# Optimization experiments

Measured on AMD Instinct MI355X. Metric: run time of the kernel, lower is better.

## Reference

```python
import jax, jax.numpy as jnp
import numpy as np

K = 8          # number of TR cores / modes
D = 1024       # categories per mode
R = 64         # TR rank
NDRAWS = 2048
EPS = 1e-30


def setup_inputs() -> dict:
    key = jax.random.key(0)
    ks = jax.random.split(key, K)
    inp = {f"log_core{i}": jax.random.normal(ks[i], (D, R, R), dtype=jnp.float32)
           for i in range(K)}
    inp["n_draws"] = NDRAWS
    return inp


def _sample(cores, n_draws, seed=1):
    """Batched version of trip_index_sample: all draws sampled in parallel."""
    k = len(cores)
    # heads[j] = S_0 @ ... @ S_{j-1} with S_i = core_i.sum(0); heads[0] = None
    heads = [None]
    acc = cores[0].sum(axis=0)
    for c in cores[1:]:
        heads.append(acc)
        acc = acc @ c.sum(axis=0)
    norm = acc  # S_0 ... S_{K-1}

    keys = jax.random.split(jax.random.key(seed), k)
    tail = None          # [B, r_{j+1}, r_K] running suffix product per draw
    idxs = []
    for step, j in enumerate(range(k - 1, -1, -1)):
        core, head = cores[j], heads[j]
        if tail is None:
            # first step (j = K-1): marginal weights shared by all draws
            if head is None:  # degenerate K == 1 case
                w = jnp.trace(core, axis1=1, axis2=2)
            else:
                w = jnp.einsum('ab,nba->n', head, core)
            ix = jax.random.categorical(keys[step], jnp.log(jnp.clip(w, EPS)),
                                        shape=(n_draws,))
            tail = core[ix]  # [B, r_j, r_K]
        else:
            # M = tail @ head : [B, r_{j+1}, r_j] (head is None only at j == 0,
            # where r_0 == r_K so tail already has the right shape)
            M = tail if head is None else tail @ head
            w = jnp.einsum('nab,Bba->Bn', core, M)  # [B, d_j]
            ix = jax.random.categorical(keys[step], jnp.log(jnp.clip(w, EPS)),
                                        axis=-1)
            tail = jnp.einsum('Bab,Bbc->Bac', core[ix], tail)
        idxs.append(ix)
    sample = jnp.stack(idxs[::-1], axis=1)  # [B, K], mode order 0..K-1
    log_p = jnp.log(jnp.clip(jnp.trace(tail, axis1=1, axis2=2), EPS)) \
            - jnp.log(jnp.trace(norm))
    return sample, log_p


def reference(log_core0, log_core1, log_core2, log_core3,
              log_core4, log_core5, log_core6, log_core7, n_draws):
    log_cores = [log_core0, log_core1, log_core2, log_core3,
                 log_core4, log_core5, log_core6, log_core7]
    cores = [jax.nn.softplus(c) for c in log_cores]
    sample, log_p = _sample(cores, n_draws)
    return sample, log_p
```

## Files before the change

kernel.cpp:

```cpp
#include <hip/hip_runtime.h>
#include <stdint.h>
#include <math.h>

#define D_CAT  1024
#define R_TR   64
#define RR     4096
#define NDRAWS 2048
#define KMODES 8

struct CorePtrs { const float* p[KMODES]; };

typedef __attribute__((ext_vector_type(8))) __bf16 bf16x8;
typedef __attribute__((ext_vector_type(4))) float  f32x4;
typedef unsigned int u32;

union BF8 { ushort u[8]; bf16x8 v; };

static __device__ inline void async_cp16(const void* g, void* l) {
  __builtin_amdgcn_global_load_lds(
      (const __attribute__((address_space(1))) u32*)g,
      (__attribute__((address_space(3))) u32*)l, 16, 0, 0);
}

static __host__ __device__ inline uint32_t rotl32(uint32_t x, int r) {
  return (x << r) | (x >> (32 - r));
}
static __host__ __device__ inline void tf2x32(uint32_t k1, uint32_t k2,
                                              uint32_t x0, uint32_t x1,
                                              uint32_t& o0, uint32_t& o1) {
  uint32_t ks0 = k1, ks1 = k2, ks2 = k1 ^ k2 ^ 0x1BD11BDAu;
  x0 += ks0; x1 += ks1;
  x0 += x1; x1 = rotl32(x1, 13); x1 ^= x0;
  x0 += x1; x1 = rotl32(x1, 15); x1 ^= x0;
  x0 += x1; x1 = rotl32(x1, 26); x1 ^= x0;
  x0 += x1; x1 = rotl32(x1, 6);  x1 ^= x0;
  x0 += ks1; x1 += ks2 + 1u;
  x0 += x1; x1 = rotl32(x1, 17); x1 ^= x0;
  x0 += x1; x1 = rotl32(x1, 29); x1 ^= x0;
  x0 += x1; x1 = rotl32(x1, 16); x1 ^= x0;
  x0 += x1; x1 = rotl32(x1, 24); x1 ^= x0;
  x0 += ks2; x1 += ks0 + 2u;
  x0 += x1; x1 = rotl32(x1, 13); x1 ^= x0;
  x0 += x1; x1 = rotl32(x1, 15); x1 ^= x0;
  x0 += x1; x1 = rotl32(x1, 26); x1 ^= x0;
  x0 += x1; x1 = rotl32(x1, 6);  x1 ^= x0;
  x0 += ks0; x1 += ks1 + 3u;
  x0 += x1; x1 = rotl32(x1, 17); x1 ^= x0;
  x0 += x1; x1 = rotl32(x1, 29); x1 ^= x0;
  x0 += x1; x1 = rotl32(x1, 16); x1 ^= x0;
  x0 += x1; x1 = rotl32(x1, 24); x1 ^= x0;
  x0 += ks1; x1 += ks2 + 4u;
  x0 += x1; x1 = rotl32(x1, 13); x1 ^= x0;
  x0 += x1; x1 = rotl32(x1, 15); x1 ^= x0;
  x0 += x1; x1 = rotl32(x1, 26); x1 ^= x0;
  x0 += x1; x1 = rotl32(x1, 6);  x1 ^= x0;
  x0 += ks2; x1 += ks0 + 5u;
  o0 = x0; o1 = x1;
}

static __device__ inline float softplus_fast(float x) {
  float e = __expf(-fabsf(x));
  return fmaxf(x, 0.0f) + __logf(1.0f + e);
}

static __device__ inline unsigned short f32_bf16(float f) {
  uint32_t u = __float_as_uint(f);
  u += 0x7fffu + ((u >> 16) & 1u);
  return (unsigned short)(u >> 16);
}

static __device__ inline float gumbel_at(uint32_t k1, uint32_t k2, uint32_t e) {
  uint32_t o0, o1;
  tf2x32(k1, k2, 0u, e, o0, o1);
  uint32_t bits = o0 ^ o1;
  float f = __uint_as_float((bits >> 9) | 0x3F800000u) - 1.0f;
  float u = (f > 0.0f) ? f : 1.17549435e-38f;
  return -logf(-logf(u));
}


__global__ void k_sentinel(float* out, int n) {
  int i = blockIdx.x * 256 + threadIdx.x;
  if (i < n) out[i] = -12288.0f;
}

__global__ __launch_bounds__(256) void k_spart(CorePtrs cp, float* __restrict__ Spart) {
  const int bid = blockIdx.x, tid = threadIdx.x;
  const int i = bid >> 8, c = bid & 255;
  const float* src = cp.p[i] + (size_t)c * 4 * RR;
  float acc[16];
#pragma unroll
  for (int k = 0; k < 16; ++k) acc[k] = 0.0f;
#pragma unroll
  for (int d = 0; d < 4; ++d) {
    const float* row = src + (size_t)d * RR;
#pragma unroll
    for (int k = 0; k < 16; ++k)
      acc[k] += softplus_fast(row[tid + k * 256]);
  }
  float* dst = Spart + (size_t)bid * RR;
#pragma unroll
  for (int k = 0; k < 16; ++k) dst[tid + k * 256] = acc[k];
}

__global__ __launch_bounds__(256) void k_sreduce(const float* __restrict__ Spart,
                                                 double* __restrict__ S) {
  const int idx = blockIdx.x * 256 + threadIdx.x;
  const int i = idx >> 12, rr = idx & 4095;
  const float* p = Spart + ((size_t)i << 20) + rr;
  double a0 = 0.0, a1 = 0.0, a2 = 0.0, a3 = 0.0;
  for (int c = 0; c < 256; c += 4) {
    a0 += (double)p[(size_t)(c + 0) * RR];
    a1 += (double)p[(size_t)(c + 1) * RR];
    a2 += (double)p[(size_t)(c + 2) * RR];
    a3 += (double)p[(size_t)(c + 3) * RR];
  }
  S[idx] = (a0 + a1) + (a2 + a3);
}

__global__ __launch_bounds__(256) void k_heads(const double* __restrict__ S,
                                               double* __restrict__ heads,
                                               double* __restrict__ misc) {
  __shared__ double cur[RR];
  __shared__ double Sm[RR];
  __shared__ double tbuf[64];
  const int tid = threadIdx.x;
  const int bcol = tid & 63;
  const int a0 = tid >> 6;
#pragma unroll
  for (int k = 0; k < 16; ++k) {
    int p = tid + k * 256;
    double v = S[p];
    cur[p] = v;
    heads[p] = v;
  }
  __syncthreads();
  for (int m = 1; m <= 6; ++m) {
#pragma unroll
    for (int k = 0; k < 16; ++k) {
      int p = tid + k * 256;
      Sm[p] = S[(size_t)m * RR + p];
    }
    __syncthreads();
    double acc[16];
#pragma unroll
    for (int k = 0; k < 16; ++k) acc[k] = 0.0;
    for (int c = 0; c < 64; ++c) {
      double s = Sm[c * 64 + bcol];
#pragma unroll
      for (int k = 0; k < 16; ++k)
        acc[k] = fma(cur[(a0 + 4 * k) * 64 + c], s, acc[k]);
    }
    __syncthreads();
#pragma unroll
    for (int k = 0; k < 16; ++k) {
      int p = tid + k * 256;
      cur[p] = acc[k];
      heads[(size_t)m * RR + p] = acc[k];
    }
    __syncthreads();
  }
#pragma unroll
  for (int k = 0; k < 16; ++k) {
    int p = tid + k * 256;
    Sm[p] = S[(size_t)7 * RR + p];
  }
  __syncthreads();
  if (tid < 64) {
    double acc = 0.0;
    for (int c = 0; c < 64; ++c)
      acc = fma(cur[tid * 64 + c], Sm[c * 64 + tid], acc);
    tbuf[tid] = acc;
  }
  __syncthreads();
  if (tid == 0) {
    double tr = 0.0;
    for (int a = 0; a < 64; ++a) tr += tbuf[a];
    misc[0] = log(tr);
  }
}

__global__ __launch_bounds__(256) void k_w0(const float* __restrict__ raw,
                                            const double* __restrict__ head7,
                                            float* __restrict__ W) {
  const int tid = threadIdx.x;
  const int lane = tid & 63;
  const int n = blockIdx.x * 4 + (tid >> 6);
  const float* crow = raw + (size_t)n * RR;
  double acc = 0.0;
  for (int q = lane; q < RR; q += 64)
    acc = fma((double)softplus_fast(crow[q]), head7[(q & 63) * 64 + (q >> 6)], acc);
  for (int m = 32; m; m >>= 1) acc += __shfl_xor(acc, m);
  if (lane == 0) W[n] = (float)acc;
}

__global__ __launch_bounds__(256) void k_spmt(const float* __restrict__ src,
                                              ushort* __restrict__ Bh,
                                              ushort* __restrict__ Bl,
                                              const float* __restrict__ tail,
                                              const double* __restrict__ head, int useHead,
                                              ushort* __restrict__ Ah,
                                              ushort* __restrict__ Al) {
  __shared__ alignas(16) float smem[4176];
  const int bid = blockIdx.x, tid = threadIdx.x;
  if (bid < 4096) {
    const size_t i4 = ((size_t)bid * 256 + tid) * 4;
    float4 v = *(const float4*)(src + i4);
    const float ov[4] = {softplus_fast(v.x), softplus_fast(v.y),
                         softplus_fast(v.z), softplus_fast(v.w)};
    ushort h4[4], l4[4];
#pragma unroll
    for (int q = 0; q < 4; ++q) {
      ushort h = f32_bf16(ov[q]);
      float hf = __uint_as_float((uint32_t)h << 16);
      h4[q] = h;
      l4[q] = f32_bf16(ov[q] - hf);
    }
    *(ushort4*)(Bh + i4) = make_ushort4(h4[0], h4[1], h4[2], h4[3]);
    *(ushort4*)(Bl + i4) = make_ushort4(l4[0], l4[1], l4[2], l4[3]);
    return;
  }
  const int blk = bid - 4096;
  if (useHead) {
    ushort (*hT)[4096] = (ushort(*)[4096])smem;
#pragma unroll
    for (int rep = 0; rep < 16; ++rep) {
      int i = tid + rep * 256;
      float v = (float)head[(i & 63) * 64 + (i >> 6)];
      ushort h = f32_bf16(v);
      float hf = __uint_as_float((uint32_t)h << 16);
      int dst = (i & 0xFC0) | (((((i >> 3) & 7) ^ ((i >> 6) & 7)) << 3)) | (i & 7);
      hT[0][dst] = h;
      hT[1][dst] = f32_bf16(v - hf);
    }
    __syncthreads();
    const int w = tid >> 6, l = tid & 63;
    const int B = blk * 4 + w;
    const float* tb = tail + (size_t)B * RR;
    const int lrow = l & 15, kg = l >> 4;
    ushort* ah_out = Ah + (size_t)B * RR;
    ushort* al_out = Al + (size_t)B * RR;
    for (int it = 0; it < 4; ++it) {
      BF8 afh[2], afl[2];
#pragma unroll
      for (int kt = 0; kt < 2; ++kt) {
        const float* s2 = tb + (it * 16 + lrow) * 64 + kt * 32 + kg * 8;
        float4 v0 = *(const float4*)s2;
        float4 v1 = *(const float4*)(s2 + 4);
        float vv[8] = {v0.x, v0.y, v0.z, v0.w, v1.x, v1.y, v1.z, v1.w};
#pragma unroll
        for (int q = 0; q < 8; ++q) {
          ushort h = f32_bf16(vv[q]);
          float hf = __uint_as_float((uint32_t)h << 16);
          afh[kt].u[q] = h;
          afl[kt].u[q] = f32_bf16(vv[q] - hf);
        }
      }
#pragma unroll
      for (int kt2 = 0; kt2 < 4; ++kt2) {
        f32x4 hh = (f32x4)0.0f, sm = (f32x4)0.0f;
#pragma unroll
        for (int kt = 0; kt < 2; ++kt) {
          int rowB = kt2 * 16 + lrow;
          int kcA  = kt * 4 + kg;
          int off  = rowB * 64 + ((kcA ^ (rowB & 7)) << 3);
          bf16x8 bh = *(const bf16x8*)&hT[0][off];
          bf16x8 bl = *(const bf16x8*)&hT[1][off];
          hh = __builtin_amdgcn_mfma_f32_16x16x32_bf16(afh[kt].v, bh, hh, 0, 0, 0);
          sm = __builtin_amdgcn_mfma_f32_16x16x32_bf16(afh[kt].v, bl, sm, 0, 0, 0);
          sm = __builtin_amdgcn_mfma_f32_16x16x32_bf16(afl[kt].v, bh, sm, 0, 0, 0);
        }
        ushort h4[4], l4[4];
#pragma unroll
        for (int q = 0; q < 4; ++q) {
          float v = hh[q] + sm[q];
          ushort h = f32_bf16(v);
          float hf = __uint_as_float((uint32_t)h << 16);
          h4[q] = h;
          l4[q] = f32_bf16(v - hf);
        }
        int o = (kt2 * 16 + lrow) * 64 + it * 16 + kg * 4;
        *(ushort4*)(ah_out + o) = make_ushort4(h4[0], h4[1], h4[2], h4[3]);
        *(ushort4*)(al_out + o) = make_ushort4(l4[0], l4[1], l4[2], l4[3]);
      }
    }
  } else {
    float* tl = smem;
    for (int d = 0; d < 4; ++d) {
      const int B = blk * 4 + d;
      const float* tb = tail + (size_t)B * RR;
      ushort* ah_out = Ah + (size_t)B * RR;
      ushort* al_out = Al + (size_t)B * RR;
      __syncthreads();
#pragma unroll
      for (int r = 0; r < 4; ++r) {
        int p = tid * 4 + r * 1024;
        int i = p >> 6, k = p & 63;
        float4 v = *(const float4*)(tb + p);
        tl[i * 65 + k + 0] = v.x; tl[i * 65 + k + 1] = v.y;
        tl[i * 65 + k + 2] = v.z; tl[i * 65 + k + 3] = v.w;
      }
      __syncthreads();
#pragma unroll
      for (int r = 0; r < 4; ++r) {
        int p = tid * 4 + r * 1024;
        int k = p >> 6, i0 = p & 63;
        ushort h4[4], l4[4];
#pragma unroll
        for (int q = 0; q < 4; ++q) {
          float m = tl[(i0 + q) * 65 + k];
          ushort h = f32_bf16(m);
          float hf = __uint_as_float((uint32_t)h << 16);
          h4[q] = h;
          l4[q] = f32_bf16(m - hf);
        }
        *(ushort4*)(ah_out + p) = make_ushort4(h4[0], h4[1], h4[2], h4[3]);
        *(ushort4*)(al_out + p) = make_ushort4(l4[0], l4[1], l4[2], l4[3]);
      }
    }
  }
}

__global__ __launch_bounds__(256) void k_wgemm(const ushort* __restrict__ Ah,
                                               const ushort* __restrict__ Al,
                                               const ushort* __restrict__ Bh,
                                               const ushort* __restrict__ Bl,
                                               float* __restrict__ W) {
  __shared__ ushort lds[4 * 4096];
  const int tid = threadIdx.x;
  const int L = blockIdx.x;
  const int half = L >> 9;
  const int r = L & 511;
  const int x = r & 7, j = r >> 3;
  const int bn = (x & 1) * 8 + (j & 7);
  const int bb = (x >> 1) * 8 + (j >> 3);
  const int w = tid >> 6, l = tid & 63;

  const int srow = l >> 3;
  const int skc  = l & 7;
  const ushort* gbase;
  {
    const ushort* bases[4] = {Ah + (size_t)bb * 64 * RR, Al + (size_t)bb * 64 * RR,
                              Bh + (size_t)bn * 64 * RR, Bl + (size_t)bn * 64 * RR};
    gbase = bases[w] + (size_t)srow * RR + (size_t)((skc ^ srow) * 8)
          + (size_t)half * 2048;
  }

  const int wm = (w >> 1) * 32, wn = (w & 1) * 32;
  const int lrow = l & 15;
  const int kg   = l >> 4;

  f32x4 acc_hh[2][2], acc_sm[2][2], hht[2][2];
#pragma unroll
  for (int mt = 0; mt < 2; ++mt)
#pragma unroll
    for (int nt = 0; nt < 2; ++nt) {
      acc_hh[mt][nt] = (f32x4)0.0f;
      acc_sm[mt][nt] = (f32x4)0.0f;
      hht[mt][nt]    = (f32x4)0.0f;
    }

  int roffA[2][2], roffB[2][2];
#pragma unroll
  for (int mt = 0; mt < 2; ++mt)
#pragma unroll
    for (int kt = 0; kt < 2; ++kt) {
      int rowA = wm + mt * 16 + lrow;
      int kcA  = kt * 4 + kg;
      roffA[mt][kt] = rowA * 64 + ((kcA ^ (rowA & 7)) << 3);
      int rowB = wn + mt * 16 + lrow;
      roffB[mt][kt] = rowB * 64 + ((kcA ^ (rowB & 7)) << 3);
    }

  for (int t = 0; t < 32; ++t) {
    __syncthreads();
#pragma unroll
    for (int q = 0; q < 8; ++q)
      async_cp16(gbase + (size_t)q * 8 * RR + t * 64, &lds[w * 4096 + q * 512]);
    __syncthreads();
#pragma unroll
    for (int kt = 0; kt < 2; ++kt) {
      bf16x8 ah[2], al[2], bh[2], bl[2];
#pragma unroll
      for (int mt = 0; mt < 2; ++mt) {
        ah[mt] = *(const bf16x8*)&lds[0 * 4096 + roffA[mt][kt]];
        al[mt] = *(const bf16x8*)&lds[1 * 4096 + roffA[mt][kt]];
      }
#pragma unroll
      for (int nt = 0; nt < 2; ++nt) {
        bh[nt] = *(const bf16x8*)&lds[2 * 4096 + roffB[nt][kt]];
        bl[nt] = *(const bf16x8*)&lds[3 * 4096 + roffB[nt][kt]];
      }
#pragma unroll
      for (int mt = 0; mt < 2; ++mt)
#pragma unroll
        for (int nt = 0; nt < 2; ++nt) {
          acc_hh[mt][nt] = __builtin_amdgcn_mfma_f32_16x16x32_bf16(ah[mt], bh[nt], acc_hh[mt][nt], 0, 0, 0);
          acc_sm[mt][nt] = __builtin_amdgcn_mfma_f32_16x16x32_bf16(ah[mt], bl[nt], acc_sm[mt][nt], 0, 0, 0);
          acc_sm[mt][nt] = __builtin_amdgcn_mfma_f32_16x16x32_bf16(al[mt], bh[nt], acc_sm[mt][nt], 0, 0, 0);
        }
    }
    if ((t & 15) == 15) {
#pragma unroll
      for (int mt = 0; mt < 2; ++mt)
#pragma unroll
        for (int nt = 0; nt < 2; ++nt) {
          hht[mt][nt] += acc_hh[mt][nt];
          acc_hh[mt][nt] = (f32x4)0.0f;
        }
    }
  }

  float* Wout = W + (size_t)half * NDRAWS * D_CAT;
#pragma unroll
  for (int mt = 0; mt < 2; ++mt)
#pragma unroll
    for (int nt = 0; nt < 2; ++nt)
#pragma unroll
      for (int q = 0; q < 4; ++q) {
        int gr = bb * 64 + wm + mt * 16 + kg * 4 + q;
        int gc = bn * 64 + wn + nt * 16 + lrow;
        Wout[(size_t)gr * D_CAT + gc] = hht[mt][nt][q] + acc_sm[mt][nt][q];
      }
}

__global__ __launch_bounds__(256) void k_samptail(const float* __restrict__ W, int shared_row,
                                                  uint32_t key1, uint32_t key2,
                                                  float* __restrict__ out, int mode_j,
                                                  const float* __restrict__ raw,
                                                  const ushort* __restrict__ Bh,
                                                  const ushort* __restrict__ Bl,
                                                  float* __restrict__ tail, int first) {
  __shared__ float sv[4];
  __shared__ int   si[4];
  __shared__ int   s_m;
  __shared__ alignas(16) ushort Th[4096];
  __shared__ alignas(16) ushort Tl[4096];
  const int b = blockIdx.x, tid = threadIdx.x;

  {
    const float* w0row = W + (shared_row ? 0 : (size_t)b * D_CAT);
    const float* w1row = W + (size_t)NDRAWS * D_CAT + (size_t)b * D_CAT;
    float best = -3.4e38f; int bidx = 0x7fffffff;
    for (int k = 0; k < 4; ++k) {
      int n = tid + k * 256;
      float wv = shared_row ? w0row[n] : (w0row[n] + w1row[n]);
      float lg = logf(fmaxf(wv, 1e-30f));
      float v = gumbel_at(key1, key2, (uint32_t)(b * D_CAT + n)) + lg;
      if (v > best || (v == best && n < bidx)) { best = v; bidx = n; }
    }
    for (int m = 32; m; m >>= 1) {
      float ov = __shfl_xor(best, m);
      int   oi = __shfl_xor(bidx, m);
      if (ov > best || (ov == best && oi < bidx)) { best = ov; bidx = oi; }
    }
    if ((tid & 63) == 0) { sv[tid >> 6] = best; si[tid >> 6] = bidx; }
    __syncthreads();
    if (tid == 0) {
      for (int t = 1; t < 4; ++t)
        if (sv[t] > best || (sv[t] == best && si[t] < bidx)) { best = sv[t]; bidx = si[t]; }
      s_m = bidx;
      out[b * KMODES + mode_j] = (float)bidx;
    }
    __syncthreads();
  }
  const int m = s_m;
  float* trow = tail + (size_t)b * RR;

  if (first) {
    const float* crow = raw + (size_t)m * RR;
#pragma unroll
    for (int r = 0; r < 4; ++r) {
      float4 v = *(const float4*)(crow + tid * 4 + r * 1024);
      float4 o;
      o.x = softplus_fast(v.x); o.y = softplus_fast(v.y);
      o.z = softplus_fast(v.z); o.w = softplus_fast(v.w);
      *(float4*)(trow + tid * 4 + r * 1024) = o;
    }
    return;
  }
  const ushort* ch = Bh + (size_t)m * RR;
  const ushort* cl = Bl + (size_t)m * RR;

#pragma unroll
  for (int r = 0; r < 4; ++r) {
    int p = tid * 4 + r * 1024;
    int i = p >> 6, k = p & 63;
    float4 v = *(const float4*)(trow + p);
    float vv[4] = {v.x, v.y, v.z, v.w};
#pragma unroll
    for (int q = 0; q < 4; ++q) {
      int row = k + q;
      int dst = row * 64 + ((((i >> 3) ^ (row & 7)) << 3)) + (i & 7);
      ushort h = f32_bf16(vv[q]);
      float hf = __uint_as_float((uint32_t)h << 16);
      Th[dst] = h;
      Tl[dst] = f32_bf16(vv[q] - hf);
    }
  }
  __syncthreads();

  const int w = tid >> 6, l = tid & 63;
  const int lrow = l & 15, kg = l >> 4;
  bf16x8 ah[2], al[2];
#pragma unroll
  for (int kt = 0; kt < 2; ++kt) {
    int off = (w * 16 + lrow) * 64 + kt * 32 + kg * 8;
    ah[kt] = *(const bf16x8*)(ch + off);
    al[kt] = *(const bf16x8*)(cl + off);
  }
#pragma unroll
  for (int jt = 0; jt < 4; ++jt) {
    f32x4 hh = (f32x4)0.0f, sm = (f32x4)0.0f;
#pragma unroll
    for (int kt = 0; kt < 2; ++kt) {
      int rowB = jt * 16 + lrow;
      int kcA  = kt * 4 + kg;
      int off  = rowB * 64 + ((kcA ^ (rowB & 7)) << 3);
      bf16x8 bh = *(const bf16x8*)&Th[off];
      bf16x8 bl = *(const bf16x8*)&Tl[off];
      hh = __builtin_amdgcn_mfma_f32_16x16x32_bf16(ah[kt], bh, hh, 0, 0, 0);
      sm = __builtin_amdgcn_mfma_f32_16x16x32_bf16(ah[kt], bl, sm, 0, 0, 0);
      sm = __builtin_amdgcn_mfma_f32_16x16x32_bf16(al[kt], bh, sm, 0, 0, 0);
      sm = __builtin_amdgcn_mfma_f32_16x16x32_bf16(al[kt], bl, sm, 0, 0, 0);
    }
#pragma unroll
    for (int q = 0; q < 4; ++q)
      trow[(w * 16 + kg * 4 + q) * 64 + jt * 16 + lrow] = hh[q] + sm[q];
  }
}

__global__ __launch_bounds__(256) void k_logp(const float* __restrict__ tail,
                                              const double* __restrict__ misc,
                                              float* __restrict__ out) {
  const int b = blockIdx.x * 256 + threadIdx.x;
  double tr = 0.0;
  for (int a = 0; a < 64; ++a) tr += (double)tail[(size_t)b * RR + a * 65];
  double lp = log(fmax(tr, 1e-30)) - misc[0];
  out[NDRAWS * KMODES + b] = (float)lp;
}

extern "C" void kernel_launch(void* const* d_in, const int* in_sizes, int n_in,
                              void* d_out, int out_size, void* d_ws, size_t ws_size,
                              hipStream_t stream) {
  (void)in_sizes; (void)n_in;
  CorePtrs cp;
  for (int i = 0; i < KMODES; ++i) cp.p[i] = (const float*)d_in[i];
  float* outf = (float*)d_out;

  char* base = (char*)d_ws;
  const size_t o_w     = 0;
  const size_t o_tail  = o_w + (size_t)2 * NDRAWS * D_CAT * 4;
  const size_t o_ahl   = o_tail + (size_t)NDRAWS * RR * 4;
  const size_t o_spart = o_ahl;
  const size_t o_S     = o_ahl + (size_t)NDRAWS * RR * 4;
  const size_t o_heads = o_S + (size_t)KMODES * RR * 8;
  const size_t o_misc  = o_heads + (size_t)7 * RR * 8;
  const size_t o_bh    = o_misc + 256;
  const size_t o_bl    = o_bh + (size_t)D_CAT * RR * 2;
  const size_t NEED    = o_bl + (size_t)D_CAT * RR * 2;
  if (ws_size < NEED) {
    k_sentinel<<<(out_size + 255) / 256, 256, 0, stream>>>(outf, out_size);
    return;
  }

  float*  W     = (float*)(base + o_w);
  float*  tail  = (float*)(base + o_tail);
  ushort* Ah    = (ushort*)(base + o_ahl);
  ushort* Al    = Ah + (size_t)NDRAWS * RR;
  float*  Spart = (float*)(base + o_spart);
  double* S     = (double*)(base + o_S);
  double* heads = (double*)(base + o_heads);
  double* misc  = (double*)(base + o_misc);
  ushort* Bh    = (ushort*)(base + o_bh);
  ushort* Bl    = (ushort*)(base + o_bl);

  uint32_t kk1[KMODES], kk2[KMODES];
  for (uint32_t s = 0; s < KMODES; ++s) tf2x32(0u, 1u, 0u, s, kk1[s], kk2[s]);

  k_spart  <<<2048, 256, 0, stream>>>(cp, Spart);
  k_sreduce<<<128,  256, 0, stream>>>(Spart, S);
  k_heads  <<<1,    256, 0, stream>>>(S, heads, misc);

  for (int s = 0; s < KMODES; ++s) {
    const int j = 7 - s;
    if (s == 0) {
      k_w0<<<256, 256, 0, stream>>>(cp.p[7], heads + (size_t)6 * RR, W);
    } else {
      k_spmt<<<4608, 256, 0, stream>>>(cp.p[j], Bh, Bl, tail,
                                       j > 0 ? heads + (size_t)(j - 1) * RR : heads,
                                       j > 0 ? 1 : 0, Ah, Al);
      k_wgemm<<<1024, 256, 0, stream>>>(Ah, Al, Bh, Bl, W);
    }
    k_samptail<<<NDRAWS, 256, 0, stream>>>(W, s == 0 ? 1 : 0, kk1[s], kk2[s],
                                           outf, j, cp.p[j], Bh, Bl, tail,
                                           s == 0 ? 1 : 0);
  }
  k_logp<<<KMODES, 256, 0, stream>>>(tail, misc, outf);
}
```

Measured before the change: 880.0 us.

## Enlarge wgemm tile to 128x64 per block to halve B-operand reloads

The split-bf16 W GEMM now gives each block a 128-row by 64-column output tile instead of 64x64. Each wave computes 4x2 MFMA tiles, and the grid shrinks from 1024 to 512 blocks. The A operand (high and low) fills 4 LDS slabs and the B operand 2, so each B tile is loaded from global memory half as often and more MFMA work is done per barrier. In exchange the kernel uses more accumulator registers and LDS per block, which may lower occupancy, and half as many blocks are available to cover the GPU's compute units.

```diff
diff --git a/kernel.cpp b/kernel.cpp
--- a/kernel.cpp
+++ b/kernel.cpp
@@ -326,33 +326,33 @@
                                                const ushort* __restrict__ Bh,
                                                const ushort* __restrict__ Bl,
                                                float* __restrict__ W) {
-  __shared__ ushort lds[4 * 4096];
+  __shared__ ushort lds[6 * 4096];
   const int tid = threadIdx.x;
   const int L = blockIdx.x;
-  const int half = L >> 9;
-  const int r = L & 511;
-  const int x = r & 7, j = r >> 3;
-  const int bn = (x & 1) * 8 + (j & 7);
-  const int bb = (x >> 1) * 8 + (j >> 3);
+  const int x = L & 7, j = L >> 3;
+  const int half = j >> 5;
+  const int j2 = j & 31;
+  const int bn = (x & 1) * 8 + (j2 & 7);
+  const int bm = (x >> 1) * 4 + (j2 >> 3);
   const int w = tid >> 6, l = tid & 63;
 
   const int srow = l >> 3;
   const int skc  = l & 7;
-  const ushort* gbase;
-  {
-    const ushort* bases[4] = {Ah + (size_t)bb * 64 * RR, Al + (size_t)bb * 64 * RR,
-                              Bh + (size_t)bn * 64 * RR, Bl + (size_t)bn * 64 * RR};
-    gbase = bases[w] + (size_t)srow * RR + (size_t)((skc ^ srow) * 8)
-          + (size_t)half * 2048;
-  }
-
-  const int wm = (w >> 1) * 32, wn = (w & 1) * 32;
+  const ushort* gbaseA = (w >= 2 ? Al : Ah) + (size_t)bm * 128 * RR
+                       + (size_t)((w & 1) * 64 + srow) * RR
+                       + (size_t)(((skc ^ srow)) * 8) + (size_t)half * 2048;
+  const ushort* gbaseB0 = Bh + (size_t)bn * 64 * RR + (size_t)srow * RR
+                        + (size_t)(((skc ^ srow)) * 8) + (size_t)half * 2048;
+  const ushort* gbaseB1 = Bl + (size_t)bn * 64 * RR + (size_t)srow * RR
+                        + (size_t)(((skc ^ srow)) * 8) + (size_t)half * 2048;
+
+  const int wm = (w >> 1) * 64, wn = (w & 1) * 32;
   const int lrow = l & 15;
   const int kg   = l >> 4;
 
-  f32x4 acc_hh[2][2], acc_sm[2][2], hht[2][2];
-#pragma unroll
-  for (int mt = 0; mt < 2; ++mt)
+  f32x4 acc_hh[4][2], acc_sm[4][2], hht[4][2];
+#pragma unroll
+  for (int mt = 0; mt < 4; ++mt)
 #pragma unroll
     for (int nt = 0; nt < 2; ++nt) {
       acc_hh[mt][nt] = (f32x4)0.0f;
@@ -360,39 +360,51 @@
       hht[mt][nt]    = (f32x4)0.0f;
     }
 
-  int roffA[2][2], roffB[2][2];
-#pragma unroll
-  for (int mt = 0; mt < 2; ++mt)
+  int roffA[4][2], roffB[2][2];
+#pragma unroll
+  for (int kt = 0; kt < 2; ++kt) {
+    int kcA = kt * 4 + kg;
+#pragma unroll
+    for (int mt = 0; mt < 4; ++mt) {
+      int rowA = wm + mt * 16 + lrow;
+      roffA[mt][kt] = rowA * 64 + ((kcA ^ (rowA & 7)) << 3);
+    }
+#pragma unroll
+    for (int nt = 0; nt < 2; ++nt) {
+      int rowB = wn + nt * 16 + lrow;
+      roffB[nt][kt] = 16384 + rowB * 64 + ((kcA ^ (rowB & 7)) << 3);
+    }
+  }
+
+  for (int t = 0; t < 32; ++t) {
+    const int koff = t * 64;
+    __syncthreads();
+#pragma unroll
+    for (int q = 0; q < 8; ++q)
+      async_cp16(gbaseA + (size_t)q * 8 * RR + koff,
+                 &lds[w * 4096 + q * 512]);
+#pragma unroll
+    for (int q = 0; q < 4; ++q) {
+      const int g = w * 4 + q;
+      const ushort* gb = (g >= 8 ? gbaseB1 : gbaseB0) + (size_t)((g & 7) * 8) * RR + koff;
+      async_cp16(gb, &lds[16384 + g * 512]);
+    }
+    __syncthreads();
 #pragma unroll
     for (int kt = 0; kt < 2; ++kt) {
-      int rowA = wm + mt * 16 + lrow;
-      int kcA  = kt * 4 + kg;
-      roffA[mt][kt] = rowA * 64 + ((kcA ^ (rowA & 7)) << 3);
-      int rowB = wn + mt * 16 + lrow;
-      roffB[mt][kt] = rowB * 64 + ((kcA ^ (rowB & 7)) << 3);
-    }
-
-  for (int t = 0; t < 32; ++t) {
-    __syncthreads();
-#pragma unroll
-    for (int q = 0; q < 8; ++q)
-      async_cp16(gbase + (size_t)q * 8 * RR + t * 64, &lds[w * 4096 + q * 512]);
-    __syncthreads();
-#pragma unroll
-    for (int kt = 0; kt < 2; ++kt) {
-      bf16x8 ah[2], al[2], bh[2], bl[2];
-#pragma unroll
-      for (int mt = 0; mt < 2; ++mt) {
-        ah[mt] = *(const bf16x8*)&lds[0 * 4096 + roffA[mt][kt]];
-        al[mt] = *(const bf16x8*)&lds[1 * 4096 + roffA[mt][kt]];
+      bf16x8 ah[4], al[4], bh[2], bl[2];
+#pragma unroll
+      for (int mt = 0; mt < 4; ++mt) {
+        ah[mt] = *(const bf16x8*)&lds[0 * 8192 + roffA[mt][kt]];
+        al[mt] = *(const bf16x8*)&lds[1 * 8192 + roffA[mt][kt]];
       }
 #pragma unroll
       for (int nt = 0; nt < 2; ++nt) {
-        bh[nt] = *(const bf16x8*)&lds[2 * 4096 + roffB[nt][kt]];
-        bl[nt] = *(const bf16x8*)&lds[3 * 4096 + roffB[nt][kt]];
+        bh[nt] = *(const bf16x8*)&lds[roffB[nt][kt]];
+        bl[nt] = *(const bf16x8*)&lds[4096 + roffB[nt][kt]];
       }
 #pragma unroll
-      for (int mt = 0; mt < 2; ++mt)
+      for (int mt = 0; mt < 4; ++mt)
 #pragma unroll
         for (int nt = 0; nt < 2; ++nt) {
           acc_hh[mt][nt] = __builtin_amdgcn_mfma_f32_16x16x32_bf16(ah[mt], bh[nt], acc_hh[mt][nt], 0, 0, 0);
@@ -402,7 +414,7 @@
     }
     if ((t & 15) == 15) {
 #pragma unroll
-      for (int mt = 0; mt < 2; ++mt)
+      for (int mt = 0; mt < 4; ++mt)
 #pragma unroll
         for (int nt = 0; nt < 2; ++nt) {
           hht[mt][nt] += acc_hh[mt][nt];
@@ -413,12 +425,12 @@
 
   float* Wout = W + (size_t)half * NDRAWS * D_CAT;
 #pragma unroll
-  for (int mt = 0; mt < 2; ++mt)
+  for (int mt = 0; mt < 4; ++mt)
 #pragma unroll
     for (int nt = 0; nt < 2; ++nt)
 #pragma unroll
       for (int q = 0; q < 4; ++q) {
-        int gr = bb * 64 + wm + mt * 16 + kg * 4 + q;
+        int gr = bm * 128 + wm + mt * 16 + kg * 4 + q;
         int gc = bn * 64 + wn + nt * 16 + lrow;
         Wout[(size_t)gr * D_CAT + gc] = hht[mt][nt][q] + acc_sm[mt][nt][q];
       }
@@ -590,7 +602,7 @@
       k_spmt<<<4608, 256, 0, stream>>>(cp.p[j], Bh, Bl, tail,
                                        j > 0 ? heads + (size_t)(j - 1) * RR : heads,
                                        j > 0 ? 1 : 0, Ah, Al);
-      k_wgemm<<<1024, 256, 0, stream>>>(Ah, Al, Bh, Bl, W);
+      k_wgemm<<<512, 256, 0, stream>>>(Ah, Al, Bh, Bl, W);
     }
     k_samptail<<<NDRAWS, 256, 0, stream>>>(W, s == 0 ? 1 : 0, kk1[s], kk2[s],
                                            outf, j, cp.p[j], Bh, Bl, tail,
```

After: 839.0 us. 4.7% less time.
